# Kernel tuning notes

Measured on AMD Instinct MI355X. Metric: run time of the kernel, lower is better.

## Reference

```python
import jax, jax.numpy as jnp
import numpy as np
from jax import lax


def conv2d(x, w):
    # NCHW conv, stride 1, SAME padding, no bias (matches conv3x3/conv1x1 bias=False)
    return lax.conv_general_dilated(x, w, (1, 1), 'SAME',
                                    dimension_numbers=('NCHW', 'OIHW', 'NCHW'))


def scan_dir(x, w, b, axis, reverse):
    # IRNN recurrence along `axis`: h[t] = relu(w*h[t-1] + b + x[t]), h[0] = x[0]
    # w, b: per-channel scalars [C] (grouped 1x1 conv)
    xs = jnp.moveaxis(x, axis, 0)  # [T, B, C, L]
    if reverse:
        xs = xs[::-1]
    wb = w[None, :, None]
    bb = b[None, :, None]

    def step(h, xt):
        h = jax.nn.relu(wb * h + bb + xt)
        return h, h

    _, ys = lax.scan(step, xs[0], xs[1:])
    out = jnp.concatenate([xs[:1], ys], axis=0)
    if reverse:
        out = out[::-1]
    return jnp.moveaxis(out, 0, axis)


def irnn(x, ws, bs):
    # ws/bs: [4, C], direction order = up, right, down, left
    up = scan_dir(x, ws[0], bs[0], 2, True)
    right = scan_dir(x, ws[1], bs[1], 3, False)
    down = scan_dir(x, ws[2], bs[2], 2, False)
    left = scan_dir(x, ws[3], bs[3], 3, True)
    return jnp.concatenate([up, right, down, left], axis=1)  # [B, 4C, H, W]


def setup_inputs() -> dict:
    key = jax.random.key(0)
    ks = jax.random.split(key, 10)
    B, C, H, W = 8, 32, 256, 256
    x = jax.random.normal(ks[0], (B, C, H, W), jnp.float32)
    conv_in_w = jax.random.normal(ks[1], (C, C, 3, 3), jnp.float32) * 0.05
    conv2_w = jax.random.normal(ks[2], (C, 4 * C, 3, 3), jnp.float32) * 0.05
    conv3_w = jax.random.normal(ks[3], (C, 4 * C, 3, 3), jnp.float32) * 0.05
    conv_out_w = jax.random.normal(ks[4], (1, C, 1, 1), jnp.float32) * 0.05
    # grouped 1x1 conv weights: small magnitude keeps the 255-step recurrence stable
    irnn1_w = jax.random.uniform(ks[5], (4, C), jnp.float32, -0.2, 0.2)
    irnn1_b = jax.random.uniform(ks[6], (4, C), jnp.float32, -0.1, 0.1)
    irnn2_w = jax.random.uniform(ks[7], (4, C), jnp.float32, -0.2, 0.2)
    irnn2_b = jax.random.uniform(ks[8], (4, C), jnp.float32, -0.1, 0.1)
    return {"x": x, "conv_in_w": conv_in_w, "conv2_w": conv2_w,
            "conv3_w": conv3_w, "conv_out_w": conv_out_w,
            "irnn1_w": irnn1_w, "irnn1_b": irnn1_b,
            "irnn2_w": irnn2_w, "irnn2_b": irnn2_b}


def reference(x, conv_in_w, conv2_w, conv3_w, conv_out_w,
              irnn1_w, irnn1_b, irnn2_w, irnn2_b):
    # NOTE: torch's attention branch uses non-in-place .mul() whose result is
    # discarded, so attention has no effect on the output; omitted here.
    out = conv2d(x, conv_in_w)                                 # [B, C, H, W]
    out = conv2d(irnn(out, irnn1_w, irnn1_b), conv2_w)         # [B, C, H, W]
    out = jax.nn.relu(conv2d(irnn(out, irnn2_w, irnn2_b), conv3_w))
    mask = jax.nn.sigmoid(conv2d(out, conv_out_w))             # [B, 1, H, W]
    return mask
```

## Files before the change

### kernel.cpp

```cpp
#include <hip/hip_runtime.h>
#include <hip/hip_bf16.h>
#include <math.h>

static constexpr int Bn = 8, Cn = 32, Hn = 256, Wn = 256;
static constexpr int HP = 258;
static constexpr size_t PLANE = (size_t)Hn * Wn;
static constexpr size_t PB = (size_t)HP * HP;

typedef __attribute__((ext_vector_type(8))) short bf16x8;
typedef __attribute__((ext_vector_type(4))) float f32x4;
typedef __attribute__((ext_vector_type(4))) short s16x4;
typedef __attribute__((ext_vector_type(4))) int   i32x4;

__device__ inline short bf16bits(float v) {
    union { __hip_bfloat16 h; short s; } u; u.h = __float2bfloat16(v);
    return u.s;
}
__device__ inline float bits2f(short s) {
    union { unsigned int u; float f; } u; u.u = ((unsigned int)(unsigned short)s) << 16;
    return u.f;
}
__device__ inline void async16(const short* g, short* l) {
    __builtin_amdgcn_global_load_lds(
        (const __attribute__((address_space(1))) unsigned int*)g,
        (__attribute__((address_space(3))) unsigned int*)l, 16, 0, 0);
}

template <int CIN>
__global__ __launch_bounds__(256) void pack_w(const float* __restrict__ w,
                                              __hip_bfloat16* __restrict__ wp)
{
    int idx = blockIdx.x * 256 + threadIdx.x;
    int j = idx & 7, gpos = (idx >> 3) & 3, m = (idx >> 5) & 15, mt = (idx >> 9) & 1;
    int rest = idx >> 10;
    int s = rest % 9, cb = rest / 9;
    int g = gpos ^ ((m >> 2) & 3);
    int co = mt * 16 + m;
    int ci = cb * 32 + g * 8 + j;
    float v = w[((size_t)(co * CIN + ci) * 3 + s / 3) * 3 + (s % 3)];
    wp[idx] = __float2bfloat16(v);
}

template <int NB>
__global__ __launch_bounds__(256) void zero_border(short* __restrict__ p)
{
    int idx = blockIdx.x * 256 + threadIdx.x;
    if (idx >= NB * 1028 * 4) return;
    int c8 = idx & 3;
    int rest = idx >> 2;
    int pe = rest % 1028, bb = rest / 1028;
    int y, x;
    if (pe < 258)      { y = 0;   x = pe; }
    else if (pe < 516) { y = 257; x = pe - 258; }
    else if (pe < 772) { y = pe - 516 + 1; x = 0; }
    else               { y = pe - 772 + 1; x = 257; }
    *(i32x4*)(p + ((size_t)bb * PB + (size_t)y * HP + x) * 32 + c8 * 8) = i32x4{};
}

__global__ __launch_bounds__(256) void x_to_nhwc(const float* __restrict__ in,
                                                 __hip_bfloat16* __restrict__ out)
{
    __shared__ unsigned int shU[32 * 17];
    unsigned short* sh16 = (unsigned short*)shU;
    int tid = threadIdx.x;
    int px0 = blockIdx.x * 32;
    int b = blockIdx.y;
    const float2* in2 = (const float2*)(in + ((size_t)b * 32) * PLANE + px0);
    for (int i = tid; i < 512; i += 256) {
        int ch = i >> 4, pxp = i & 15;
        float2 v = in2[(size_t)ch * (PLANE / 2) + pxp];
        unsigned int lo = (unsigned short)bf16bits(v.x);
        unsigned int hi = (unsigned short)bf16bits(v.y);
        shU[ch * 17 + pxp] = lo | (hi << 16);
    }
    __syncthreads();
    int yy = px0 >> 8, xx0 = px0 & 255;
    unsigned int* out32 = (unsigned int*)out
        + ((size_t)b * PB + (size_t)(yy + 1) * HP + xx0 + 1) * 16;
    for (int i = tid; i < 512; i += 256) {
        int px = i >> 4, chp = i & 15;
        unsigned int v = (unsigned int)sh16[(2 * chp) * 34 + px]
                       | ((unsigned int)sh16[(2 * chp + 1) * 34 + px] << 16);
        out32[(size_t)px * 16 + chp] = v;
    }
}

template <int CIN, bool RELU, bool FUSE>
__global__ __launch_bounds__(256, 4) void conv_mfma(const __hip_bfloat16* __restrict__ in,
        const __hip_bfloat16* __restrict__ wp, __hip_bfloat16* __restrict__ outA,
        const float* __restrict__ wo, float* __restrict__ outF)
{
    constexpr int CB = CIN / 32;
    constexpr int SLAB = 10880;
    constexpr int WSL  = 9216;
    constexpr int BUF  = SLAB + WSL;
    __shared__ short sIn[BUF];
    int tid = threadIdx.x;
    int lane = tid & 63, wave = tid >> 6;
    int m = lane & 15, g = lane >> 4;
    int x0 = blockIdx.x * 32, y0 = blockIdx.y * 8, b = blockIdx.z;

    const short* inS = (const short*)in;
    const short* wpS = (const short*)wp;
    f32x4 acc[2][2][2] = {};

    auto slab_src = [&](int c, int cb) -> const short* {
        int gpos = c & 3, q = c >> 2;
        int xx = q % 34, yy = q / 34;
        int gl = gpos ^ ((xx >> 2) & 3);
        return inS
            + ((size_t)(cb * 8 + b) * PB + (size_t)(y0 + yy) * HP + x0 + xx) * 32
            + gl * 8;
    };

    auto stage = [&](int cb) {
        short* dst = sIn;
        #pragma unroll
        for (int r = 0; r < 5; ++r) {
            int i = r * 256 + tid;
            async16(slab_src(i, cb), dst + (r * 256 + wave * 64) * 8);
        }
        if (wave < 2) {
            int base = 1280 + wave * 16;
            async16(slab_src(base + lane, cb), dst + base * 8);
        }
        #pragma unroll
        for (int r = 0; r < 5; ++r) {
            int i = r * 256 + tid;
            if (r < 4 || i < 1152) {
                const short* gp = wpS + (size_t)cb * WSL + i * 8;
                async16(gp, dst + SLAB + (r * 256 + wave * 64) * 8);
            }
        }
    };

    int wfoff = (m * 4 + (g ^ ((m >> 2) & 3))) * 8;

    stage(0);
    for (int cb = 0; cb < CB; ++cb) {
        __syncthreads();
        const short* sb = sIn;
        const short* sw = sb + SLAB;

        #pragma unroll
        for (int dxr = 0; dxr < 3; ++dxr) {
            int xx = m + dxr;
            const short* colp = sb + xx * 32 + (g ^ ((xx >> 2) & 3)) * 8;
            bf16x8 Bf[4][2];
            #pragma unroll
            for (int rr = 0; rr < 4; ++rr) {
                const short* rp = colp + (wave * 2 + rr) * (34 * 32);
                Bf[rr][0] = *(const bf16x8*)rp;
                Bf[rr][1] = *(const bf16x8*)(rp + 16 * 32);
            }
            #pragma unroll
            for (int dyi = 0; dyi < 3; ++dyi) {
                int s = dyi * 3 + dxr;
                bf16x8 wf0 = *(const bf16x8*)(sw + s * 1024 + wfoff);
                bf16x8 wf1 = *(const bf16x8*)(sw + s * 1024 + 512 + wfoff);
                #pragma unroll
                for (int wy = 0; wy < 2; ++wy) {
                    int rr = wy + dyi;
                    acc[wy][0][0] = __builtin_amdgcn_mfma_f32_16x16x32_bf16(wf0, Bf[rr][0], acc[wy][0][0], 0, 0, 0);
                    acc[wy][1][0] = __builtin_amdgcn_mfma_f32_16x16x32_bf16(wf1, Bf[rr][0], acc[wy][1][0], 0, 0, 0);
                    acc[wy][0][1] = __builtin_amdgcn_mfma_f32_16x16x32_bf16(wf0, Bf[rr][1], acc[wy][0][1], 0, 0, 0);
                    acc[wy][1][1] = __builtin_amdgcn_mfma_f32_16x16x32_bf16(wf1, Bf[rr][1], acc[wy][1][1], 0, 0, 0);
                }
            }
        }
        if (cb + 1 < CB) {
            __syncthreads();
            stage(cb + 1);
        }
    }

    if (FUSE) {
        float wv[2][4];
        #pragma unroll
        for (int mt = 0; mt < 2; ++mt)
            #pragma unroll
            for (int r = 0; r < 4; ++r) wv[mt][r] = wo[mt * 16 + g * 4 + r];
        #pragma unroll
        for (int wy = 0; wy < 2; ++wy) {
            int y = y0 + wave * 2 + wy;
            #pragma unroll
            for (int nt = 0; nt < 2; ++nt) {
                float s = 0.f;
                #pragma unroll
                for (int mt = 0; mt < 2; ++mt)
                    #pragma unroll
                    for (int r = 0; r < 4; ++r)
                        s = fmaf(fmaxf(acc[wy][mt][nt][r], 0.f), wv[mt][r], s);
                s += __shfl_xor(s, 16);
                s += __shfl_xor(s, 32);
                if (g == 0)
                    outF[(size_t)(b * 256 + y) * 256 + x0 + nt * 16 + m]
                        = 1.f / (1.f + expf(-s));
            }
        }
    } else {
        short* outS = (short*)outA;
        #pragma unroll
        for (int wy = 0; wy < 2; ++wy) {
            int y = y0 + wave * 2 + wy;
            #pragma unroll
            for (int nt = 0; nt < 2; ++nt) {
                int x = x0 + nt * 16 + m;
                size_t base = ((size_t)((b * 256 + y) * 256 + x)) * 32;
                #pragma unroll
                for (int mt = 0; mt < 2; ++mt) {
                    int co = mt * 16 + g * 4;
                    s16x4 ov;
                    #pragma unroll
                    for (int r = 0; r < 4; ++r) {
                        float v = acc[wy][mt][nt][r];
                        if (RELU) v = fmaxf(v, 0.f);
                        ov[r] = bf16bits(v);
                    }
                    *(s16x4*)(outS + base + co) = ov;
                }
            }
        }
    }
}

__global__ __launch_bounds__(256) void irnn_vert(const __hip_bfloat16* __restrict__ A,
        const float* __restrict__ w4, const float* __restrict__ b4,
        __hip_bfloat16* __restrict__ I)
{
    __shared__ short sA[64 * 256];
    int tid = threadIdx.x;
    int c = tid & 31, xo = tid >> 5;
    int x = blockIdx.x * 8 + xo;
    int y1 = blockIdx.y * 32;
    int b = blockIdx.z;
    const short* aS = (const short*)A;

    for (int i = tid; i < 2048; i += 256) {
        int slot = i >> 5, c8 = i & 31;
        int y = y1 - 16 + slot;
        if ((unsigned)y < (unsigned)Hn) {
            const short* gp = aS + ((size_t)(b * 256 + y) * 256 + blockIdx.x * 8) * 32 + c8 * 8;
            *(i32x4*)(sA + slot * 256 + c8 * 8) = *(const i32x4*)gp;
        }
    }
    __syncthreads();

    float wd = w4[64 + c], bd = b4[64 + c];
    float wu = w4[c],      bu = b4[c];
    short* od = (short*)I + ((size_t)(2 * 8 + b) * PB + (size_t)HP + 1 + x) * 32 + c;
    short* ou = (short*)I + ((size_t)(0 * 8 + b) * PB + (size_t)HP + 1 + x) * 32 + c;
    const size_t os = (size_t)HP * 32;

    {
        int ys = y1 ? y1 - 16 : 0;
        float h = bits2f(sA[(ys - y1 + 16) * 256 + tid]);
        if (ys == y1) od[(size_t)y1 * os] = bf16bits(h);
        #pragma unroll 8
        for (int y = ys + 1; y < y1 + 32; ++y) {
            float xv = bits2f(sA[(y - y1 + 16) * 256 + tid]);
            h = fmaxf(fmaf(wd, h, bd + xv), 0.f);
            if (y >= y1) od[(size_t)y * os] = bf16bits(h);
        }
    }
    {
        int ye = (y1 + 47 > 255) ? 255 : y1 + 47;
        float h = bits2f(sA[(ye - y1 + 16) * 256 + tid]);
        if (ye == y1 + 31) ou[(size_t)ye * os] = bf16bits(h);
        #pragma unroll 8
        for (int y = ye - 1; y >= y1; --y) {
            float xv = bits2f(sA[(y - y1 + 16) * 256 + tid]);
            h = fmaxf(fmaf(wu, h, bu + xv), 0.f);
            if (y <= y1 + 31) ou[(size_t)y * os] = bf16bits(h);
        }
    }
}

__global__ __launch_bounds__(256) void irnn_horiz(const __hip_bfloat16* __restrict__ A,
        const float* __restrict__ w4, const float* __restrict__ b4,
        __hip_bfloat16* __restrict__ I)
{
    __shared__ short sA[8 * 64 * 32];
    int tid = threadIdx.x;
    int c = tid & 31, yo = tid >> 5;
    int y = blockIdx.x * 8 + yo;
    int x1 = blockIdx.y * 32;
    int b = blockIdx.z;
    const short* aS = (const short*)A;

    for (int i = tid; i < 2048; i += 256) {
        int yy = i >> 8, rem = i & 255;
        int slot = rem >> 2, c16 = rem & 3;
        int x = x1 - 16 + slot;
        if ((unsigned)x < (unsigned)Wn) {
            const short* gp = aS + ((size_t)(b * 256 + blockIdx.x * 8 + yy) * 256 + x) * 32 + c16 * 8;
            *(i32x4*)(sA + (yy * 64 + slot) * 32 + c16 * 8) = *(const i32x4*)gp;
        }
    }
    __syncthreads();

    float wr = w4[32 + c], br = b4[32 + c];
    float wl = w4[96 + c], bl = b4[96 + c];
    short* orr = (short*)I + ((size_t)(1 * 8 + b) * PB + (size_t)(1 + y) * HP + 1) * 32 + c;
    short* ol  = (short*)I + ((size_t)(3 * 8 + b) * PB + (size_t)(1 + y) * HP + 1) * 32 + c;
    const short* sRow = sA + yo * 64 * 32 + c;

    {
        int xs = x1 ? x1 - 16 : 0;
        float h = bits2f(sRow[(xs - x1 + 16) * 32]);
        if (xs == x1) orr[(size_t)x1 * 32] = bf16bits(h);
        #pragma unroll 8
        for (int x = xs + 1; x < x1 + 32; ++x) {
            float xv = bits2f(sRow[(x - x1 + 16) * 32]);
            h = fmaxf(fmaf(wr, h, br + xv), 0.f);
            if (x >= x1) orr[(size_t)x * 32] = bf16bits(h);
        }
    }
    {
        int xe = (x1 + 47 > 255) ? 255 : x1 + 47;
        float h = bits2f(sRow[(xe - x1 + 16) * 32]);
        if (xe == x1 + 31) ol[(size_t)xe * 32] = bf16bits(h);
        #pragma unroll 8
        for (int x = xe - 1; x >= x1; --x) {
            float xv = bits2f(sRow[(x - x1 + 16) * 32]);
            h = fmaxf(fmaf(wl, h, bl + xv), 0.f);
            if (x <= x1 + 31) ol[(size_t)x * 32] = bf16bits(h);
        }
    }
}

extern "C" void kernel_launch(void* const* d_in, const int* in_sizes, int n_in,
                              void* d_out, int out_size, void* d_ws, size_t ws_size,
                              hipStream_t stream)
{
    const float* x    = (const float*)d_in[0];
    const float* w_in = (const float*)d_in[1];
    const float* w2   = (const float*)d_in[2];
    const float* w3   = (const float*)d_in[3];
    const float* wo   = (const float*)d_in[4];
    const float* i1w  = (const float*)d_in[5];
    const float* i1b  = (const float*)d_in[6];
    const float* i2w  = (const float*)d_in[7];
    const float* i2b  = (const float*)d_in[8];
    float* out = (float*)d_out;

    char* ws = (char*)d_ws;
    __hip_bfloat16* Ipad  = (__hip_bfloat16*)ws;
    __hip_bfloat16* xTpad = (__hip_bfloat16*)ws;
    __hip_bfloat16* A = (__hip_bfloat16*)(ws + ((size_t)137 << 20));
    __hip_bfloat16* wp1 = (__hip_bfloat16*)(ws + ((size_t)170 << 20));
    __hip_bfloat16* wp2 = (__hip_bfloat16*)(ws + ((size_t)170 << 20) + ((size_t)1 << 19));
    __hip_bfloat16* wp3 = (__hip_bfloat16*)(ws + ((size_t)170 << 20) + ((size_t)2 << 19));

    dim3 convGrid(8, 32, 8);
    dim3 irnnGrid(32, 8, 8);

    pack_w<32> <<<36,  256, 0, stream>>>(w_in, wp1);
    pack_w<128><<<144, 256, 0, stream>>>(w2, wp2);
    pack_w<128><<<144, 256, 0, stream>>>(w3, wp3);

    zero_border<32><<<514, 256, 0, stream>>>((short*)Ipad);
    x_to_nhwc<<<dim3(2048, 8), 256, 0, stream>>>(x, xTpad);
    conv_mfma<32, false, false><<<convGrid, 256, 0, stream>>>(xTpad, wp1, A, nullptr, nullptr);

    irnn_vert <<<irnnGrid, 256, 0, stream>>>(A, i1w, i1b, Ipad);
    irnn_horiz<<<irnnGrid, 256, 0, stream>>>(A, i1w, i1b, Ipad);
    conv_mfma<128, false, false><<<convGrid, 256, 0, stream>>>(Ipad, wp2, A, nullptr, nullptr);

    irnn_vert <<<irnnGrid, 256, 0, stream>>>(A, i2w, i2b, Ipad);
    irnn_horiz<<<irnnGrid, 256, 0, stream>>>(A, i2w, i2b, Ipad);
    conv_mfma<128, true, true><<<convGrid, 256, 0, stream>>>(Ipad, wp3, nullptr, wo, out);
}
```

Measured before the change: 306.8 us.

## Merge IRNN kernels into one direction-per-block scan with 4-channel vector lanes

Replaces the separate vertical and horizontal IRNN kernels, which staged windows in LDS, with one kernel that assigns a direction per block via blockIdx.z. Each thread scans 4 channels with vectorized 8-byte global loads and stores directly. This removes the shared-memory staging, the barrier and one launch, and raises per-thread ILP. The trade-off is uncached direct global loads on a serial dependency chain and fewer threads per line.

```diff
diff --git a/kernel.cpp b/kernel.cpp
--- a/kernel.cpp
+++ b/kernel.cpp
@@ -224,107 +224,72 @@
     }
 }
 
-__global__ __launch_bounds__(256) void irnn_vert(const __hip_bfloat16* __restrict__ A,
+__global__ __launch_bounds__(256) void irnn_scan(const __hip_bfloat16* __restrict__ A,
         const float* __restrict__ w4, const float* __restrict__ b4,
         __hip_bfloat16* __restrict__ I)
 {
-    __shared__ short sA[64 * 256];
     int tid = threadIdx.x;
-    int c = tid & 31, xo = tid >> 5;
-    int x = blockIdx.x * 8 + xo;
-    int y1 = blockIdx.y * 32;
-    int b = blockIdx.z;
+    int c4 = tid & 7, lo = tid >> 3;
+    int c0 = c4 * 4;
+    int zz = blockIdx.z;
+    int dir = zz >> 3, b = zz & 7;
+    int line = blockIdx.x * 32 + lo;
+    int s1 = blockIdx.y * 32;
+    bool vert = (dir & 1) == 0;
+    bool fwd  = (dir == 1 || dir == 2);
+
     const short* aS = (const short*)A;
-
-    for (int i = tid; i < 2048; i += 256) {
-        int slot = i >> 5, c8 = i & 31;
-        int y = y1 - 16 + slot;
-        if ((unsigned)y < (unsigned)Hn) {
-            const short* gp = aS + ((size_t)(b * 256 + y) * 256 + blockIdx.x * 8) * 32 + c8 * 8;
-            *(i32x4*)(sA + slot * 256 + c8 * 8) = *(const i32x4*)gp;
-        }
-    }
-    __syncthreads();
-
-    float wd = w4[64 + c], bd = b4[64 + c];
-    float wu = w4[c],      bu = b4[c];
-    short* od = (short*)I + ((size_t)(2 * 8 + b) * PB + (size_t)HP + 1 + x) * 32 + c;
-    short* ou = (short*)I + ((size_t)(0 * 8 + b) * PB + (size_t)HP + 1 + x) * 32 + c;
-    const size_t os = (size_t)HP * 32;
-
-    {
-        int ys = y1 ? y1 - 16 : 0;
-        float h = bits2f(sA[(ys - y1 + 16) * 256 + tid]);
-        if (ys == y1) od[(size_t)y1 * os] = bf16bits(h);
+    size_t abase, astep;
+    if (vert) { abase = ((size_t)(b * 256) * 256 + line) * 32 + c0; astep = 256 * 32; }
+    else      { abase = ((size_t)(b * 256 + line) * 256) * 32 + c0; astep = 32; }
+
+    float4 wv = *(const float4*)(w4 + dir * 32 + c0);
+    float4 bv = *(const float4*)(b4 + dir * 32 + c0);
+
+    short* op; size_t ostep;
+    if (vert) { op = (short*)I + ((size_t)(dir * 8 + b) * PB + HP + 1 + line) * 32 + c0;
+                ostep = (size_t)HP * 32; }
+    else      { op = (short*)I + ((size_t)(dir * 8 + b) * PB + (size_t)(1 + line) * HP + 1) * 32 + c0;
+                ostep = 32; }
+
+    float h0, h1, h2, h3;
+    auto ld = [&](int t) -> s16x4 {
+        return *(const s16x4*)(aS + abase + (size_t)t * astep);
+    };
+    auto st = [&](int t) {
+        s16x4 ov;
+        ov[0] = bf16bits(h0); ov[1] = bf16bits(h1);
+        ov[2] = bf16bits(h2); ov[3] = bf16bits(h3);
+        *(s16x4*)(op + (size_t)t * ostep) = ov;
+    };
+
+    if (fwd) {
+        int ss = s1 ? s1 - 16 : 0;
+        s16x4 v = ld(ss);
+        h0 = bits2f(v[0]); h1 = bits2f(v[1]); h2 = bits2f(v[2]); h3 = bits2f(v[3]);
+        if (ss == s1) st(s1);
         #pragma unroll 8
-        for (int y = ys + 1; y < y1 + 32; ++y) {
-            float xv = bits2f(sA[(y - y1 + 16) * 256 + tid]);
-            h = fmaxf(fmaf(wd, h, bd + xv), 0.f);
-            if (y >= y1) od[(size_t)y * os] = bf16bits(h);
-        }
-    }
-    {
-        int ye = (y1 + 47 > 255) ? 255 : y1 + 47;
-        float h = bits2f(sA[(ye - y1 + 16) * 256 + tid]);
-        if (ye == y1 + 31) ou[(size_t)ye * os] = bf16bits(h);
+        for (int t = ss + 1; t < s1 + 32; ++t) {
+            v = ld(t);
+            h0 = fmaxf(fmaf(wv.x, h0, bv.x + bits2f(v[0])), 0.f);
+            h1 = fmaxf(fmaf(wv.y, h1, bv.y + bits2f(v[1])), 0.f);
+            h2 = fmaxf(fmaf(wv.z, h2, bv.z + bits2f(v[2])), 0.f);
+            h3 = fmaxf(fmaf(wv.w, h3, bv.w + bits2f(v[3])), 0.f);
+            if (t >= s1) st(t);
+        }
+    } else {
+        int se = (s1 + 47 > 255) ? 255 : s1 + 47;
+        s16x4 v = ld(se);
+        h0 = bits2f(v[0]); h1 = bits2f(v[1]); h2 = bits2f(v[2]); h3 = bits2f(v[3]);
+        if (se == s1 + 31) st(se);
         #pragma unroll 8
-        for (int y = ye - 1; y >= y1; --y) {
-            float xv = bits2f(sA[(y - y1 + 16) * 256 + tid]);
-            h = fmaxf(fmaf(wu, h, bu + xv), 0.f);
-            if (y <= y1 + 31) ou[(size_t)y * os] = bf16bits(h);
-        }
-    }
-}
-
-__global__ __launch_bounds__(256) void irnn_horiz(const __hip_bfloat16* __restrict__ A,
-        const float* __restrict__ w4, const float* __restrict__ b4,
-        __hip_bfloat16* __restrict__ I)
-{
-    __shared__ short sA[8 * 64 * 32];
-    int tid = threadIdx.x;
-    int c = tid & 31, yo = tid >> 5;
-    int y = blockIdx.x * 8 + yo;
-    int x1 = blockIdx.y * 32;
-    int b = blockIdx.z;
-    const short* aS = (const short*)A;
-
-    for (int i = tid; i < 2048; i += 256) {
-        int yy = i >> 8, rem = i & 255;
-        int slot = rem >> 2, c16 = rem & 3;
-        int x = x1 - 16 + slot;
-        if ((unsigned)x < (unsigned)Wn) {
-            const short* gp = aS + ((size_t)(b * 256 + blockIdx.x * 8 + yy) * 256 + x) * 32 + c16 * 8;
-            *(i32x4*)(sA + (yy * 64 + slot) * 32 + c16 * 8) = *(const i32x4*)gp;
-        }
-    }
-    __syncthreads();
-
-    float wr = w4[32 + c], br = b4[32 + c];
-    float wl = w4[96 + c], bl = b4[96 + c];
-    short* orr = (short*)I + ((size_t)(1 * 8 + b) * PB + (size_t)(1 + y) * HP + 1) * 32 + c;
-    short* ol  = (short*)I + ((size_t)(3 * 8 + b) * PB + (size_t)(1 + y) * HP + 1) * 32 + c;
-    const short* sRow = sA + yo * 64 * 32 + c;
-
-    {
-        int xs = x1 ? x1 - 16 : 0;
-        float h = bits2f(sRow[(xs - x1 + 16) * 32]);
-        if (xs == x1) orr[(size_t)x1 * 32] = bf16bits(h);
-        #pragma unroll 8
-        for (int x = xs + 1; x < x1 + 32; ++x) {
-            float xv = bits2f(sRow[(x - x1 + 16) * 32]);
-            h = fmaxf(fmaf(wr, h, br + xv), 0.f);
-            if (x >= x1) orr[(size_t)x * 32] = bf16bits(h);
-        }
-    }
-    {
-        int xe = (x1 + 47 > 255) ? 255 : x1 + 47;
-        float h = bits2f(sRow[(xe - x1 + 16) * 32]);
-        if (xe == x1 + 31) ol[(size_t)xe * 32] = bf16bits(h);
-        #pragma unroll 8
-        for (int x = xe - 1; x >= x1; --x) {
-            float xv = bits2f(sRow[(x - x1 + 16) * 32]);
-            h = fmaxf(fmaf(wl, h, bl + xv), 0.f);
-            if (x <= x1 + 31) ol[(size_t)x * 32] = bf16bits(h);
+        for (int t = se - 1; t >= s1; --t) {
+            v = ld(t);
+            h0 = fmaxf(fmaf(wv.x, h0, bv.x + bits2f(v[0])), 0.f);
+            h1 = fmaxf(fmaf(wv.y, h1, bv.y + bits2f(v[1])), 0.f);
+            h2 = fmaxf(fmaf(wv.z, h2, bv.z + bits2f(v[2])), 0.f);
+            h3 = fmaxf(fmaf(wv.w, h3, bv.w + bits2f(v[3])), 0.f);
+            if (t <= s1 + 31) st(t);
         }
     }
 }
@@ -353,7 +318,7 @@
     __hip_bfloat16* wp3 = (__hip_bfloat16*)(ws + ((size_t)170 << 20) + ((size_t)2 << 19));
 
     dim3 convGrid(8, 32, 8);
-    dim3 irnnGrid(32, 8, 8);
+    dim3 scanGrid(8, 8, 32);
 
     pack_w<32> <<<36,  256, 0, stream>>>(w_in, wp1);
     pack_w<128><<<144, 256, 0, stream>>>(w2, wp2);
@@ -363,11 +328,9 @@
     x_to_nhwc<<<dim3(2048, 8), 256, 0, stream>>>(x, xTpad);
     conv_mfma<32, false, false><<<convGrid, 256, 0, stream>>>(xTpad, wp1, A, nullptr, nullptr);
 
-    irnn_vert <<<irnnGrid, 256, 0, stream>>>(A, i1w, i1b, Ipad);
-    irnn_horiz<<<irnnGrid, 256, 0, stream>>>(A, i1w, i1b, Ipad);
+    irnn_scan<<<scanGrid, 256, 0, stream>>>(A, i1w, i1b, Ipad);
     conv_mfma<128, false, false><<<convGrid, 256, 0, stream>>>(Ipad, wp2, A, nullptr, nullptr);
 
-    irnn_vert <<<irnnGrid, 256, 0, stream>>>(A, i2w, i2b, Ipad);
-    irnn_horiz<<<irnnGrid, 256, 0, stream>>>(A, i2w, i2b, Ipad);
+    irnn_scan<<<scanGrid, 256, 0, stream>>>(A, i2w, i2b, Ipad);
     conv_mfma<128, true, true><<<convGrid, 256, 0, stream>>>(Ipad, wp3, nullptr, wo, out);
 }
```

New measurement: 307.4 us. Within noise of the previous version (+0.2%).
